# Kernel optimization log

Hardware: AMD Instinct MI355X
Metric: run time of the kernel (lower is better)

Reference implementation:

```python
import jax, jax.numpy as jnp
import numpy as np

ORDER = 2
K = 5
CIN = 16
COUT = 16
GRID = 3  # SO(3) grid size per Euler angle (m, l, n)
EPS = 1e-16


def _constants():
    """Replicates _compute_spherical_coords_and_masks, spherical_harmonics (real SH, l<2),
    basis_functions einsum and wigner index construction from the torch module."""
    center = (K - 1) // 2
    t = center + 1
    k_max = (t - 1) ** 2 * 3
    coords = np.zeros((K, K, K, 3), np.float32)
    rad_list, masks = [], []
    for i in range(K):
        for j in range(K):
            for k in range(K):
                i1, j1, k1 = i - center, j - center, k - center
                if i1 == 0 and j1 == 0 and k1 == 0:
                    coords[i, j, k, 1] = 0.0
                    coords[i, j, k, 2] = 0.0
                    coords[i, j, k, 0] = -1.0
                else:
                    r2 = float(i1 * i1 + j1 * j1 + k1 * k1)
                    coords[i, j, k, 0] = 2.0 * r2 / k_max - 1.0
                    coords[i, j, k, 1] = np.arctan2(np.sqrt(i1 * i1 + j1 * j1), k1)
                    coords[i, j, k, 2] = np.arctan2(j1, i1)
                rv = coords[i, j, k, 0]
                if rv not in rad_list:
                    rad_list.append(rv)
                    masks.append(np.zeros((K, K, K), np.float32))
                    m = len(rad_list) - 1
                else:
                    m = rad_list.index(rv)
                masks[m][i, j, k] = 1.0
    masks = np.stack(masks[::-1], axis=0)  # (R, K, K, K)
    theta = coords[..., 1]
    phi = coords[..., 2]
    C0 = 0.28209479177387814  # Y_0^0
    C1 = 0.4886025119029199   # sqrt(3/(4*pi)) for l=1 real SH
    sph = np.stack([
        np.full((K, K, K), C0, np.float32),
        C1 * np.sin(theta) * np.sin(phi),
        C1 * np.cos(theta),
        C1 * np.sin(theta) * np.cos(phi),
    ], axis=0).astype(np.float32)  # (order^2, K, K, K)
    sph[1:, center, center, center] = 0.0  # order > 1 zeroing
    wig = []
    for l in range(ORDER):
        for i in range((2 * l + 1) ** 2):
            wig.append([l, l ** 2 + i // (2 * l + 1), l ** 2 + i % (2 * l + 1)])
    wig = np.array(wig, np.int32)  # (S, 3), S = 10 for order=2
    bf = np.einsum('rijk,lijk->lrijk', masks, sph).astype(np.float32)  # (order^2, R, K, K, K)
    return bf, wig


def setup_inputs() -> dict:
    key = jax.random.key(0)
    ks = jax.random.split(key, 6)
    bf, wig = _constants()
    R = bf.shape[1]  # 10
    S = wig.shape[0]  # 10
    return {
        'x': jax.random.normal(ks[0], (2, CIN, 40, 40, 40), jnp.float32),
        'weight': jax.random.normal(ks[1], (ORDER ** 2, R - 1, CIN, COUT), jnp.float32) * 0.1,
        'zeroweight': jax.random.normal(ks[2], (CIN, COUT), jnp.float32) * 0.1,
        'bias': jnp.zeros((COUT,), jnp.float32),
        'so3basisgrid': jax.random.normal(ks[3], (GRID, GRID, GRID, S), jnp.float32) * 0.5,
        'w_i': jax.random.uniform(ks[4], (GRID,), jnp.float32) + 0.5,
        'basis_functions': jnp.asarray(bf),
        'wig_w': jnp.asarray(wig[:, 1]),
        'wig_b': jnp.asarray(wig[:, 2]),
    }


def reference(x, weight, zeroweight, bias, so3basisgrid, w_i, basis_functions, wig_w, wig_b):
    S = wig_w.shape[0]
    B = x.shape[0]
    # zeroweight extension: (order^2, 1, Cin, Cout), nonzero only at l-index 0
    zero_ext = jnp.concatenate(
        [zeroweight[None, None], jnp.zeros((ORDER ** 2 - 1, 1, CIN, COUT), weight.dtype)], axis=0)
    wfull = jnp.concatenate([zero_ext, weight], axis=1)  # (order^2, R, Cin, Cout)
    wg = wfull[wig_w]              # (S, R, Cin, Cout)
    bg = basis_functions[wig_b]    # (S, R, K, K, K)
    # kernel synthesis; reshape exactly as torch: (S, Cin, Cout, K,K,K) -> (S*Cout, Cin, K,K,K)
    kern = jnp.einsum('lred,lrijk->ledijk', wg, bg).reshape(-1, CIN, K, K, K)
    conv = jax.lax.conv_general_dilated(
        x, kern, window_strides=(1, 1, 1), padding='VALID',
        dimension_numbers=('NCDHW', 'OIDHW', 'NCDHW'))
    conv_r = conv.reshape(B, S, COUT, *conv.shape[2:])  # (B, S, Cout, X, Y, Z)
    so3 = jnp.einsum('bsdxyz,mlns->mlnbdxyz', conv_r, so3basisgrid)
    so3 = jax.nn.relu(so3)
    wib = w_i[None, :, None, None, None, None, None, None]
    denom = jnp.sum(so3 * wib, axis=(0, 1, 2), keepdims=True) + EPS
    out = jnp.sum(so3 * (so3 / denom) * wib, axis=(0, 1, 2))  # (B, Cout, X, Y, Z)
    return out + bias[None, :, None, None, None]
```

## Files before the change

kernel.cpp:

```cpp
#include <hip/hip_runtime.h>


__global__ void prep_kernel(const float* __restrict__ weight,
                            const float* __restrict__ zw,
                            const float* __restrict__ bf,
                            float* __restrict__ W2,
                            float* __restrict__ TAB)
{
    int t = blockIdx.x * 256 + threadIdx.x;
    if (t < 10240) {
        int w = t & 3;
        int e = (t >> 2) & 15;
        int k = (t >> 6) % 20;
        int p = t / 1280;
        int r = k >> 1, di = k & 1, d = 2 * p + di;
        float v;
        if (r == 0) v = (w == 0) ? zw[e * 16 + d] : 0.f;
        else        v = weight[((w * 9 + (r - 1)) * 16 + e) * 16 + d];
        W2[t] = v;
    } else if (t < 10240 + 400) {
        int q = t - 10240;
        int l = q / 100;
        int rem = q % 100;
        int slice = rem / 4, qq = rem & 3;
        float s;
        if (qq == 3) {
            s = (l == 2) ? -1.f : 1.f;
        } else {
            s = 0.f;
            int tap = slice * 5 + qq;
            for (int r = 0; r < 10; ++r) s += bf[(l * 10 + r) * 125 + tap];
        }
        TAB[q] = s;
    }
}

__global__ __launch_bounds__(192) void fused_kernel(
    const float* __restrict__ x,
    const float* __restrict__ W2,
    const float* __restrict__ TAB,
    const float* __restrict__ g,
    const float* __restrict__ w_i,
    const float* __restrict__ bias,
    float* __restrict__ out)
{
    __shared__ float Y2[7680];
    __shared__ float CT[400];
    __shared__ float XT[3232];

    const int tid = threadIdx.x;

    const int bid  = blockIdx.x;
    const int wgid = (bid & 7) * 243 + (bid >> 3);
    const int xo  = wgid % 36;
    const int yoq = (wgid / 36) % 9;
    const int zs  = (wgid / 324) % 3;
    const int bb  = wgid / 972;

    const int s_zt = tid >> 6;
    const int lane = tid & 63;
    const int s_sd = lane >> 4;
    const int s_l  = (lane >> 2) & 3;
    const int s_yo = lane & 3;
    const int c_e  = tid & 7;
    const int c_yo = (tid >> 3) & 3;
    const int c_zt = tid / 32;

    for (int idx = tid; idx < 400; idx += 192) CT[idx] = TAB[idx];

    constexpr int RANKT[13] = {0, 1, 2, 3, 4, 5, 6, 0, 7, 8, 0, 0, 9};

    float acc[10][2][2];
    #pragma unroll
    for (int s = 0; s < 10; ++s)
        #pragma unroll
        for (int ee = 0; ee < 2; ++ee) { acc[s][ee][0] = 0.f; acc[s][ee][1] = 0.f; }

    const int s1b  = s_sd & 1;
    const int kb   = (s_sd >> 1) * 20 + s1b;
    const int wb0  = s_zt * 32 + s_yo * 4 + s_l;
    const int offa = s1b ? 16 : 0;
    const int offb = 16 - offa;
    const int ybA  = (c_zt >> 1) * 32 + (c_zt & 1) * 16 + c_yo * 4;
    const int ybB  = ybA ^ 16;

    int xtoff[4], goff[4];
    #pragma unroll
    for (int q = 0; q < 4; ++q) {
        const int idx = tid + 192 * q;
        const int j  = idx & 7;
        const int zq = (idx >> 3) & 3;
        const int ii = (idx >> 5) % 5;
        const int sd = idx / 160;
        xtoff[q] = sd * 808 + (ii * 8 + j) * 20 + 4 * zq;
        goff[q]  = sd * 64000 + ((xo + ii) * 40 + yoq * 4 + j) * 40
                   + zs * 12 + 4 * zq;
    }
    const bool has3 = tid < 64;
    const float* xbase = x + bb * 1024000;

    {
        float4 v0 = *(const float4*)(xbase + goff[0]);
        float4 v1 = *(const float4*)(xbase + goff[1]);
        float4 v2 = *(const float4*)(xbase + goff[2]);
        float4 v3 = has3 ? *(const float4*)(xbase + goff[3])
                         : make_float4(0.f, 0.f, 0.f, 0.f);
        *(float4*)(XT + xtoff[0]) = v0;
        *(float4*)(XT + xtoff[1]) = v1;
        *(float4*)(XT + xtoff[2]) = v2;
        if (has3) *(float4*)(XT + xtoff[3]) = v3;
    }
    float4 pre[4];
    {
        const float* b1 = xbase + 256000;
        pre[0] = *(const float4*)(b1 + goff[0]);
        pre[1] = *(const float4*)(b1 + goff[1]);
        pre[2] = *(const float4*)(b1 + goff[2]);
        pre[3] = has3 ? *(const float4*)(b1 + goff[3])
                      : make_float4(0.f, 0.f, 0.f, 0.f);
    }

    for (int pp = 0; pp < 4; ++pp) {
        __syncthreads();
        {
            float yreg[10][4];
            #pragma unroll
            for (int r = 0; r < 10; ++r) {
                yreg[r][0] = 0.f; yreg[r][1] = 0.f;
                yreg[r][2] = 0.f; yreg[r][3] = 0.f;
            }
            const float* xt  = XT + s_sd * 808 + 4 * s_zt;
            const float* ctp = CT + s_l * 100;
            #pragma unroll
            for (int i = 0; i < 5; ++i) {
                #pragma unroll
                for (int j = 0; j < 5; ++j) {
                    const float* rp = xt + (i * 8 + s_yo + j) * 20;
                    const float4 xa = *(const float4*)rp;
                    const float4 xb = *(const float4*)(rp + 4);
                    const float xv[8] = {xa.x, xa.y, xa.z, xa.w,
                                         xb.x, xb.y, xb.z, xb.w};
                    const float4 cc = *(const float4*)(ctp + (i * 5 + j) * 4);
                    const int dij = (i - 2) * (i - 2) + (j - 2) * (j - 2);
                    const int r04 = RANKT[dij + 4];
                    const int r13 = RANKT[dij + 1];
                    const int r2c = RANKT[dij];
                    #pragma unroll
                    for (int zz = 0; zz < 4; ++zz) {
                        const float t04 = fmaf(cc.w, xv[zz + 4], xv[zz]);
                        const float t13 = fmaf(cc.w, xv[zz + 3], xv[zz + 1]);
                        yreg[r04][zz] = fmaf(cc.x, t04, yreg[r04][zz]);
                        yreg[r13][zz] = fmaf(cc.y, t13, yreg[r13][zz]);
                        yreg[r2c][zz] = fmaf(cc.z, xv[zz + 2], yreg[r2c][zz]);
                    }
                }
            }
            #pragma unroll
            for (int r = 0; r < 10; ++r) {
                const int w0 = (kb + 2 * r) * 192 + wb0;
                Y2[w0 + offa]      = yreg[r][0];
                Y2[w0 + offa + 96] = yreg[r][1];
                Y2[w0 + offb]      = yreg[r][2];
                Y2[w0 + offb + 96] = yreg[r][3];
            }
        }
        __syncthreads();
        if (pp < 3) {
            *(float4*)(XT + xtoff[0]) = pre[0];
            *(float4*)(XT + xtoff[1]) = pre[1];
            *(float4*)(XT + xtoff[2]) = pre[2];
            if (has3) *(float4*)(XT + xtoff[3]) = pre[3];
            if (pp < 2) {
                const float* bn = xbase + (pp + 2) * 256000;
                pre[0] = *(const float4*)(bn + goff[0]);
                pre[1] = *(const float4*)(bn + goff[1]);
                pre[2] = *(const float4*)(bn + goff[2]);
                if (has3) pre[3] = *(const float4*)(bn + goff[3]);
            }
        }
        {
            const float* W2p = W2 + pp * 2560 + c_e * 8;
            #pragma unroll
            for (int k = 0; k < 40; ++k) {
                const float4 wv0 = *(const float4*)(W2p + k * 64);
                const float4 wv1 = *(const float4*)(W2p + k * 64 + 4);
                const float* yb = Y2 + k * 192 + ((k & 1) ? ybB : ybA);
                const float4 yz0 = *(const float4*)(yb);
                const float4 yz1 = *(const float4*)(yb + 96);
                {
                    acc[0][0][0] = fmaf(wv0.x, yz0.x, acc[0][0][0]);
                    acc[0][0][1] = fmaf(wv0.x, yz1.x, acc[0][0][1]);
                    acc[0][1][0] = fmaf(wv1.x, yz0.x, acc[0][1][0]);
                    acc[0][1][1] = fmaf(wv1.x, yz1.x, acc[0][1][1]);
                }
                #pragma unroll
                for (int b = 1; b < 4; ++b) {
                    const float y0 = (b == 1) ? yz0.y : (b == 2) ? yz0.z : yz0.w;
                    const float y1 = (b == 1) ? yz1.y : (b == 2) ? yz1.z : yz1.w;
                    #pragma unroll
                    for (int w = 1; w < 4; ++w) {
                        const int s = 1 + (w - 1) * 3 + (b - 1);
                        const float w0 = (w == 1) ? wv0.y : ((w == 2) ? wv0.z : wv0.w);
                        const float w1 = (w == 1) ? wv1.y : ((w == 2) ? wv1.z : wv1.w);
                        acc[s][0][0] = fmaf(w0, y0, acc[s][0][0]);
                        acc[s][0][1] = fmaf(w0, y1, acc[s][0][1]);
                        acc[s][1][0] = fmaf(w1, y0, acc[s][1][0]);
                        acc[s][1][1] = fmaf(w1, y1, acc[s][1][1]);
                    }
                }
            }
        }
    }

    const float wi0 = w_i[0], wi1 = w_i[1], wi2 = w_i[2];
    float num[2][2], den[2][2];
    #pragma unroll
    for (int ee = 0; ee < 2; ++ee) { num[ee][0] = num[ee][1] = 0.f; den[ee][0] = den[ee][1] = 0.f; }
    #pragma unroll
    for (int q = 0; q < 27; ++q) {
        const float wl = ((q / 3) % 3 == 0) ? wi0 : (((q / 3) % 3 == 1) ? wi1 : wi2);
        float gv[10];
        #pragma unroll
        for (int s = 0; s < 10; ++s) gv[s] = g[q * 10 + s];
        #pragma unroll
        for (int ee = 0; ee < 2; ++ee) {
            #pragma unroll
            for (int zi = 0; zi < 2; ++zi) {
                float v = 0.f;
                #pragma unroll
                for (int s = 0; s < 10; ++s) v = fmaf(acc[s][ee][zi], gv[s], v);
                v = fmaxf(v, 0.f);
                den[ee][zi] = fmaf(v, wl, den[ee][zi]);
                num[ee][zi] = fmaf(v * v, wl, num[ee][zi]);
            }
        }
    }
    #pragma unroll
    for (int ee = 0; ee < 2; ++ee) {
        const int e = 2 * c_e + ee;
        const float bz = bias[e];
        float* op = out + (((bb * 16 + e) * 36 + xo) * 36 + (yoq * 4 + c_yo)) * 36
                        + zs * 12 + 2 * c_zt;
        *(float2*)op = make_float2(num[ee][0] / (den[ee][0] + 1e-16f) + bz,
                                   num[ee][1] / (den[ee][1] + 1e-16f) + bz);
    }
}

extern "C" void kernel_launch(void* const* d_in, const int* in_sizes, int n_in,
                              void* d_out, int out_size, void* d_ws, size_t ws_size,
                              hipStream_t stream) {
    const float* x          = (const float*)d_in[0];
    const float* weight     = (const float*)d_in[1];
    const float* zeroweight = (const float*)d_in[2];
    const float* bias       = (const float*)d_in[3];
    const float* g          = (const float*)d_in[4];
    const float* w_i        = (const float*)d_in[5];
    const float* bf         = (const float*)d_in[6];
    float* outp = (float*)d_out;

    float* W2  = (float*)d_ws;
    float* TAB = (float*)d_ws + 10240;

    prep_kernel<<<42, 256, 0, stream>>>(weight, zeroweight, bf, W2, TAB);
    fused_kernel<<<1944, 192, 0, stream>>>(x, W2, TAB, g, w_i, bias, outp);
}
```

Baseline: 153.1 us.

## Split per-pass spatial stage into two halves to halve Y2 shared buffer

Each input-channel pass is now split into two sub-passes. In each one, a thread computes 2 z outputs over one of two channel sub-groups instead of 4 z outputs over all of them. The Y2 shared-memory staging buffer shrinks by half and the per-thread yreg array drops from 40 to 20 floats. The aim is lower LDS and register pressure so more workgroups fit per CU. The cost is twice as many barriers and re-reading overlapping x rows from LDS with narrower float2 loads.

Measured after the change: 332.1 us. +116.9%, slower.

```diff
diff --git a/kernel.cpp b/kernel.cpp
--- a/kernel.cpp
+++ b/kernel.cpp
@@ -44,7 +44,7 @@
     const float* __restrict__ bias,
     float* __restrict__ out)
 {
-    __shared__ float Y2[7680];
+    __shared__ float Y2[3840];
     __shared__ float CT[400];
     __shared__ float XT[3232];
 
@@ -57,11 +57,10 @@
     const int zs  = (wgid / 324) % 3;
     const int bb  = wgid / 972;
 
-    const int s_zt = tid >> 6;
-    const int lane = tid & 63;
-    const int s_sd = lane >> 4;
-    const int s_l  = (lane >> 2) & 3;
-    const int s_yo = lane & 3;
+    const int s_zt = tid >> 5;
+    const int sdl  = (tid >> 4) & 1;
+    const int s_l  = (tid >> 2) & 3;
+    const int s_yo = tid & 3;
     const int c_e  = tid & 7;
     const int c_yo = (tid >> 3) & 3;
     const int c_zt = tid / 32;
@@ -76,13 +75,10 @@
         #pragma unroll
         for (int ee = 0; ee < 2; ++ee) { acc[s][ee][0] = 0.f; acc[s][ee][1] = 0.f; }
 
-    const int s1b  = s_sd & 1;
-    const int kb   = (s_sd >> 1) * 20 + s1b;
-    const int wb0  = s_zt * 32 + s_yo * 4 + s_l;
-    const int offa = s1b ? 16 : 0;
-    const int offb = 16 - offa;
-    const int ybA  = (c_zt >> 1) * 32 + (c_zt & 1) * 16 + c_yo * 4;
-    const int ybB  = ybA ^ 16;
+    const int wb0 = (s_zt >> 1) * 32 + ((s_zt & 1) ^ sdl) * 16
+                  + s_yo * 4 + s_l;
+    const int ybA = (c_zt >> 1) * 32 + (c_zt & 1) * 16 + c_yo * 4;
+    const int ybB = ybA ^ 16;
 
     int xtoff[4], goff[4];
     #pragma unroll
@@ -121,91 +117,95 @@
     }
 
     for (int pp = 0; pp < 4; ++pp) {
-        __syncthreads();
-        {
-            float yreg[10][4];
-            #pragma unroll
-            for (int r = 0; r < 10; ++r) {
-                yreg[r][0] = 0.f; yreg[r][1] = 0.f;
-                yreg[r][2] = 0.f; yreg[r][3] = 0.f;
-            }
-            const float* xt  = XT + s_sd * 808 + 4 * s_zt;
-            const float* ctp = CT + s_l * 100;
-            #pragma unroll
-            for (int i = 0; i < 5; ++i) {
-                #pragma unroll
-                for (int j = 0; j < 5; ++j) {
-                    const float* rp = xt + (i * 8 + s_yo + j) * 20;
-                    const float4 xa = *(const float4*)rp;
-                    const float4 xb = *(const float4*)(rp + 4);
-                    const float xv[8] = {xa.x, xa.y, xa.z, xa.w,
-                                         xb.x, xb.y, xb.z, xb.w};
-                    const float4 cc = *(const float4*)(ctp + (i * 5 + j) * 4);
-                    const int dij = (i - 2) * (i - 2) + (j - 2) * (j - 2);
-                    const int r04 = RANKT[dij + 4];
-                    const int r13 = RANKT[dij + 1];
-                    const int r2c = RANKT[dij];
+        #pragma unroll
+        for (int h = 0; h < 2; ++h) {
+            __syncthreads();
+            {
+                const int s_sd = 2 * h + sdl;
+                float yreg[10][2];
+                #pragma unroll
+                for (int r = 0; r < 10; ++r) { yreg[r][0] = 0.f; yreg[r][1] = 0.f; }
+                const float* xt  = XT + s_sd * 808 + 2 * s_zt;
+                const float* ctp = CT + s_l * 100;
+                #pragma unroll
+                for (int i = 0; i < 5; ++i) {
                     #pragma unroll
-                    for (int zz = 0; zz < 4; ++zz) {
-                        const float t04 = fmaf(cc.w, xv[zz + 4], xv[zz]);
-                        const float t13 = fmaf(cc.w, xv[zz + 3], xv[zz + 1]);
-                        yreg[r04][zz] = fmaf(cc.x, t04, yreg[r04][zz]);
-                        yreg[r13][zz] = fmaf(cc.y, t13, yreg[r13][zz]);
-                        yreg[r2c][zz] = fmaf(cc.z, xv[zz + 2], yreg[r2c][zz]);
+                    for (int j = 0; j < 5; ++j) {
+                        const float* rp = xt + (i * 8 + s_yo + j) * 20;
+                        const float2 A = *(const float2*)(rp);
+                        const float2 B = *(const float2*)(rp + 2);
+                        const float2 C = *(const float2*)(rp + 4);
+                        const float4 cc = *(const float4*)(ctp + (i * 5 + j) * 4);
+                        const int dij = (i - 2) * (i - 2) + (j - 2) * (j - 2);
+                        const int r04 = RANKT[dij + 4];
+                        const int r13 = RANKT[dij + 1];
+                        const int r2c = RANKT[dij];
+                        {
+                            const float t04 = fmaf(cc.w, C.x, A.x);
+                            const float t13 = fmaf(cc.w, B.y, A.y);
+                            yreg[r04][0] = fmaf(cc.x, t04, yreg[r04][0]);
+                            yreg[r13][0] = fmaf(cc.y, t13, yreg[r13][0]);
+                            yreg[r2c][0] = fmaf(cc.z, B.x, yreg[r2c][0]);
+                        }
+                        {
+                            const float t04 = fmaf(cc.w, C.y, A.y);
+                            const float t13 = fmaf(cc.w, C.x, B.x);
+                            yreg[r04][1] = fmaf(cc.x, t04, yreg[r04][1]);
+                            yreg[r13][1] = fmaf(cc.y, t13, yreg[r13][1]);
+                            yreg[r2c][1] = fmaf(cc.z, B.y, yreg[r2c][1]);
+                        }
                     }
                 }
-            }
-            #pragma unroll
-            for (int r = 0; r < 10; ++r) {
-                const int w0 = (kb + 2 * r) * 192 + wb0;
-                Y2[w0 + offa]      = yreg[r][0];
-                Y2[w0 + offa + 96] = yreg[r][1];
-                Y2[w0 + offb]      = yreg[r][2];
-                Y2[w0 + offb + 96] = yreg[r][3];
-            }
-        }
-        __syncthreads();
-        if (pp < 3) {
-            *(float4*)(XT + xtoff[0]) = pre[0];
-            *(float4*)(XT + xtoff[1]) = pre[1];
-            *(float4*)(XT + xtoff[2]) = pre[2];
-            if (has3) *(float4*)(XT + xtoff[3]) = pre[3];
-            if (pp < 2) {
-                const float* bn = xbase + (pp + 2) * 256000;
-                pre[0] = *(const float4*)(bn + goff[0]);
-                pre[1] = *(const float4*)(bn + goff[1]);
-                pre[2] = *(const float4*)(bn + goff[2]);
-                if (has3) pre[3] = *(const float4*)(bn + goff[3]);
-            }
-        }
-        {
-            const float* W2p = W2 + pp * 2560 + c_e * 8;
-            #pragma unroll
-            for (int k = 0; k < 40; ++k) {
-                const float4 wv0 = *(const float4*)(W2p + k * 64);
-                const float4 wv1 = *(const float4*)(W2p + k * 64 + 4);
-                const float* yb = Y2 + k * 192 + ((k & 1) ? ybB : ybA);
-                const float4 yz0 = *(const float4*)(yb);
-                const float4 yz1 = *(const float4*)(yb + 96);
-                {
-                    acc[0][0][0] = fmaf(wv0.x, yz0.x, acc[0][0][0]);
-                    acc[0][0][1] = fmaf(wv0.x, yz1.x, acc[0][0][1]);
-                    acc[0][1][0] = fmaf(wv1.x, yz0.x, acc[0][1][0]);
-                    acc[0][1][1] = fmaf(wv1.x, yz1.x, acc[0][1][1]);
-                }
-                #pragma unroll
-                for (int b = 1; b < 4; ++b) {
-                    const float y0 = (b == 1) ? yz0.y : (b == 2) ? yz0.z : yz0.w;
-                    const float y1 = (b == 1) ? yz1.y : (b == 2) ? yz1.z : yz1.w;
+                #pragma unroll
+                for (int r = 0; r < 10; ++r) {
+                    const int w0 = (2 * r + sdl) * 192 + wb0;
+                    Y2[w0]      = yreg[r][0];
+                    Y2[w0 + 96] = yreg[r][1];
+                }
+            }
+            __syncthreads();
+            if (h == 1 && pp < 3) {
+                *(float4*)(XT + xtoff[0]) = pre[0];
+                *(float4*)(XT + xtoff[1]) = pre[1];
+                *(float4*)(XT + xtoff[2]) = pre[2];
+                if (has3) *(float4*)(XT + xtoff[3]) = pre[3];
+                if (pp < 2) {
+                    const float* bn = xbase + (pp + 2) * 256000;
+                    pre[0] = *(const float4*)(bn + goff[0]);
+                    pre[1] = *(const float4*)(bn + goff[1]);
+                    pre[2] = *(const float4*)(bn + goff[2]);
+                    if (has3) pre[3] = *(const float4*)(bn + goff[3]);
+                }
+            }
+            {
+                const float* W2p = W2 + (2 * pp + h) * 1280 + c_e * 8;
+                #pragma unroll
+                for (int k = 0; k < 20; ++k) {
+                    const float4 wv0 = *(const float4*)(W2p + k * 64);
+                    const float4 wv1 = *(const float4*)(W2p + k * 64 + 4);
+                    const float* yb = Y2 + k * 192 + ((k & 1) ? ybB : ybA);
+                    const float4 yz0 = *(const float4*)(yb);
+                    const float4 yz1 = *(const float4*)(yb + 96);
+                    {
+                        acc[0][0][0] = fmaf(wv0.x, yz0.x, acc[0][0][0]);
+                        acc[0][0][1] = fmaf(wv0.x, yz1.x, acc[0][0][1]);
+                        acc[0][1][0] = fmaf(wv1.x, yz0.x, acc[0][1][0]);
+                        acc[0][1][1] = fmaf(wv1.x, yz1.x, acc[0][1][1]);
+                    }
                     #pragma unroll
-                    for (int w = 1; w < 4; ++w) {
-                        const int s = 1 + (w - 1) * 3 + (b - 1);
-                        const float w0 = (w == 1) ? wv0.y : ((w == 2) ? wv0.z : wv0.w);
-                        const float w1 = (w == 1) ? wv1.y : ((w == 2) ? wv1.z : wv1.w);
-                        acc[s][0][0] = fmaf(w0, y0, acc[s][0][0]);
-                        acc[s][0][1] = fmaf(w0, y1, acc[s][0][1]);
-                        acc[s][1][0] = fmaf(w1, y0, acc[s][1][0]);
-                        acc[s][1][1] = fmaf(w1, y1, acc[s][1][1]);
+                    for (int b = 1; b < 4; ++b) {
+                        const float y0 = (b == 1) ? yz0.y : (b == 2) ? yz0.z : yz0.w;
+                        const float y1 = (b == 1) ? yz1.y : (b == 2) ? yz1.z : yz1.w;
+                        #pragma unroll
+                        for (int w = 1; w < 4; ++w) {
+                            const int s = 1 + (w - 1) * 3 + (b - 1);
+                            const float w0 = (w == 1) ? wv0.y : ((w == 2) ? wv0.z : wv0.w);
+                            const float w1 = (w == 1) ? wv1.y : ((w == 2) ? wv1.z : wv1.w);
+                            acc[s][0][0] = fmaf(w0, y0, acc[s][0][0]);
+                            acc[s][0][1] = fmaf(w0, y1, acc[s][0][1]);
+                            acc[s][1][0] = fmaf(w1, y0, acc[s][1][0]);
+                            acc[s][1][1] = fmaf(w1, y1, acc[s][1][1]);
+                        }
                     }
                 }
             }
```
